# Kernel tuning notes

Measured on AMD Instinct MI355X. Metric: run time of the kernel, lower is better.

## Reference

```python
import jax, jax.numpy as jnp
import numpy as np

EPS = 1e-6
N_LEVELS = 8
BASE_RES = 16
DESIRED_RES = 128
N_POINTS = 524288


def _grid_meta():
    # replicate DAGrid.__init__ level resolutions and flat-table offsets
    b = (DESIRED_RES / BASE_RES) ** (1.0 / (N_LEVELS - 1))
    scales, offsets = [], [0]
    for i in range(N_LEVELS):
        res = int(BASE_RES * b ** i)
        scales.append(res)
        offsets.append(offsets[-1] + (res + 1) ** 3)
    return scales, offsets


def setup_inputs() -> dict:
    key = jax.random.key(0)
    scales, offsets = _grid_meta()
    lo = np.array([-1.0, -1.0, -1.0], np.float32)
    hi_eps = np.array([1.0, 1.0, 1.0], np.float32) - EPS  # bounds[1] -= eps before anchor init
    anchors = []
    for res in scales:
        axes = [np.linspace(lo[d], hi_eps[d], res + 1, dtype=np.float32) for d in range(3)]
        g = np.stack(np.meshgrid(*axes, indexing='ij'), axis=-1).reshape(-1, 3)
        anchors.append(g)
    data = jnp.asarray(np.concatenate(anchors, axis=0))  # (T, 3) learned grid param
    xyz = jax.random.normal(key, (N_POINTS, 3), dtype=jnp.float32)
    return {
        'xyz': xyz,
        'data': data,
        'scales': jnp.asarray(scales, jnp.float32),              # (L,)
        'level_offsets': jnp.asarray(offsets[:-1], jnp.int32),   # (L,)
        'bounds': jnp.asarray(np.stack([lo, np.array([1.0, 1.0, 1.0], np.float32)])),  # (2,3) raw bbox
    }


def reference(xyz, data, scales, level_offsets, bounds):
    L = scales.shape[0]
    lo = bounds[0]
    hi = bounds[1] - EPS
    size = jnp.max(bounds[1] - bounds[0])
    x = jnp.clip(xyz, lo, hi)
    xn = (x - lo) / size                                   # (N,3) in [0,1)
    fx = xn[None, :, :] * scales[:, None, None]            # (L,N,3)
    base = jnp.floor(fx).astype(jnp.int32)                 # (L,N,3) lower corner
    off = fx - base.astype(fx.dtype)                       # (L,N,3) trilinear frac
    corners = jnp.asarray([[0, 0, 0], [0, 0, 1], [0, 1, 0], [0, 1, 1],
                           [1, 0, 0], [1, 0, 1], [1, 1, 0], [1, 1, 1]], jnp.int32)  # (8,3)
    idx = base[:, :, None, :] + corners[None, None, :, :]  # (L,N,8,3)
    r1 = (scales + 1.0).astype(jnp.int32)                  # (L,) points per axis
    ind = (idx[..., 0] * (r1 * r1)[:, None, None]
           + idx[..., 1] * r1[:, None, None]
           + idx[..., 2]
           + level_offsets[:, None, None])                 # (L,N,8) flat gather index
    val = data[ind]                                        # (L,N,8,3) gathered anchors
    cf = corners.astype(fx.dtype)
    w = jnp.clip(1.0 - cf + (2.0 * cf - 1.0) * off[:, :, None, :], 0.0, 1.0)  # (L,N,8,3)
    w = w[..., 0] * w[..., 1] * w[..., 2]                  # (L,N,8) trilinear weights
    freqs = (2.0 ** jnp.arange(L, dtype=fx.dtype))[:, None, None, None]
    enc = jnp.concatenate([jnp.sin(val * freqs), jnp.cos(val * freqs)], axis=-1)  # (L,N,8,6)
    out = jnp.einsum('lnk,lnkf->nlf', w, enc)              # (N,L,6)
    out = out.reshape(xyz.shape[0], -1)                    # (N, 6*L)
    return jnp.concatenate([xyz, out], axis=-1)            # (N, 3 + 6*L)
```

## Files before the change

kernel.cpp:

```cpp
#include <hip/hip_runtime.h>

#define NLEV 8
#define PTS_PER_BLOCK 32
#define ROW_F 51

__global__ __launch_bounds__(256) void dagrid_kernel(
    const float* __restrict__ xyz,
    const float* __restrict__ data,
    const float* __restrict__ scales,
    const int*   __restrict__ level_offsets,
    const float* __restrict__ bounds,
    float* __restrict__ out,
    int npts)
{
    __shared__ float sxyz[PTS_PER_BLOCK * 3];
    __shared__ float sres[PTS_PER_BLOCK][ROW_F];

    const int tid = threadIdx.x;
    const int l   = tid & 7;
    const int p   = tid >> 3;
    const int block_base = blockIdx.x * PTS_PER_BLOCK;

    if (tid < PTS_PER_BLOCK * 3) {
        int gi = block_base * 3 + tid;
        sxyz[tid] = (gi < npts * 3) ? xyz[gi] : 0.0f;
    }
    __syncthreads();

    const int n = block_base + p;
    const bool active = (n < npts);

    const float lox = bounds[0], loy = bounds[1], loz = bounds[2];
    const float hix = bounds[3] - 1e-6f;
    const float hiy = bounds[4] - 1e-6f;
    const float hiz = bounds[5] - 1e-6f;
    const float size = fmaxf(fmaxf(bounds[3] - bounds[0], bounds[4] - bounds[1]),
                             bounds[5] - bounds[2]);
    const float inv_size = 1.0f / size;

    const float rx = sxyz[p * 3 + 0];
    const float ry = sxyz[p * 3 + 1];
    const float rz = sxyz[p * 3 + 2];

    float acc0 = 0.f, acc1 = 0.f, acc2 = 0.f, acc3 = 0.f, acc4 = 0.f, acc5 = 0.f;

    if (active) {
        const float x = fminf(fmaxf(rx, lox), hix);
        const float y = fminf(fmaxf(ry, loy), hiy);
        const float z = fminf(fmaxf(rz, loz), hiz);
        const float xn = (x - lox) * inv_size;
        const float yn = (y - loy) * inv_size;
        const float zn = (z - loz) * inv_size;

        const float scale = scales[l];
        const int off_l = level_offsets[l];
        const int r1 = (int)scale + 1;
        const int r1sq = r1 * r1;

        const float fx = xn * scale;
        const float fy = yn * scale;
        const float fz = zn * scale;
        const float bxf = floorf(fx);
        const float byf = floorf(fy);
        const float bzf = floorf(fz);
        const int bx = (int)bxf;
        const int by = (int)byf;
        const int bz = (int)bzf;
        const float ox = fx - bxf;
        const float oy = fy - byf;
        const float oz = fz - bzf;

        const int i000 = bx * r1sq + by * r1 + bz + off_l;
        const float freq = (float)(1 << l);
        const float w_z0 = 1.0f - oz;

        #pragma unroll
        for (int cx = 0; cx < 2; ++cx) {
            const float wx = cx ? ox : (1.0f - ox);
            #pragma unroll
            for (int cy = 0; cy < 2; ++cy) {
                const float wxy = wx * (cy ? oy : (1.0f - oy));
                const float w0 = wxy * w_z0;
                const float w1 = wxy * oz;
                const float* pv = data + 3 * (size_t)(i000 + cx * r1sq + cy * r1);
                const float v0x = pv[0], v0y = pv[1], v0z = pv[2];
                const float v1x = pv[3], v1y = pv[4], v1z = pv[5];

                float a;
                a = v0x * freq; acc0 += w0 * __sinf(a); acc3 += w0 * __cosf(a);
                a = v0y * freq; acc1 += w0 * __sinf(a); acc4 += w0 * __cosf(a);
                a = v0z * freq; acc2 += w0 * __sinf(a); acc5 += w0 * __cosf(a);
                a = v1x * freq; acc0 += w1 * __sinf(a); acc3 += w1 * __cosf(a);
                a = v1y * freq; acc1 += w1 * __sinf(a); acc4 += w1 * __cosf(a);
                a = v1z * freq; acc2 += w1 * __sinf(a); acc5 += w1 * __cosf(a);
            }
        }
    }

    {
        float* row = sres[p];
        const int c = 3 + l * 6;
        row[c + 0] = acc0; row[c + 1] = acc1; row[c + 2] = acc2;
        row[c + 3] = acc3; row[c + 4] = acc4; row[c + 5] = acc5;
        if (l == 0) { row[0] = rx; row[1] = ry; row[2] = rz; }
    }
    __syncthreads();

    {
        const float* flat = &sres[0][0];
        float* ob = out + (size_t)block_base * ROW_F;
        const int lim = npts * ROW_F - block_base * ROW_F;
        for (int i = tid; i < PTS_PER_BLOCK * ROW_F; i += 256) {
            if (i < lim) ob[i] = flat[i];
        }
    }
}

extern "C" void kernel_launch(void* const* d_in, const int* in_sizes, int n_in,
                              void* d_out, int out_size, void* d_ws, size_t ws_size,
                              hipStream_t stream) {
    const float* xyz           = (const float*)d_in[0];
    const float* data          = (const float*)d_in[1];
    const float* scales        = (const float*)d_in[2];
    const int*   level_offsets = (const int*)d_in[3];
    const float* bounds        = (const float*)d_in[4];
    float* out = (float*)d_out;

    const int npts = in_sizes[0] / 3;
    const int nblocks = (npts + PTS_PER_BLOCK - 1) / PTS_PER_BLOCK;
    dagrid_kernel<<<nblocks, 256, 0, stream>>>(xyz, data, scales, level_offsets,
                                               bounds, out, npts);
}
```

Baseline: 144.3 us.

## Repack grid table to float4 rows and vectorize gathers and output stores

Adds a pre-pass kernel that copies the (T,3) anchor table into a padded float4 table in workspace, so each corner pair is fetched with two 16-byte loads instead of six scalar loads. The main kernel also vectorizes the xyz load and the output store for full blocks, and uses sincos in place of separate sin and cos calls. The cost is an extra kernel launch plus a full read and write of the table (about 1.2M entries) on every call. The original scalar path is kept as a fallback for when no workspace is provided.

```diff
diff --git a/kernel.cpp b/kernel.cpp
--- a/kernel.cpp
+++ b/kernel.cpp
@@ -4,7 +4,153 @@
 #define PTS_PER_BLOCK 32
 #define ROW_F 51
 
+__global__ __launch_bounds__(256) void repack_kernel(
+    const float* __restrict__ data, float4* __restrict__ tab, int T)
+{
+    const int g = blockIdx.x * 256 + threadIdx.x;
+    const int base = g * 4;
+    if (base >= T) return;
+    if (base + 4 <= T) {
+        const float4* src = (const float4*)(data + (size_t)base * 3);
+        const float4 a = src[0], b = src[1], c = src[2];
+        tab[base + 0] = make_float4(a.x, a.y, a.z, 0.f);
+        tab[base + 1] = make_float4(a.w, b.x, b.y, 0.f);
+        tab[base + 2] = make_float4(b.z, b.w, c.x, 0.f);
+        tab[base + 3] = make_float4(c.y, c.z, c.w, 0.f);
+    } else {
+        for (int j = base; j < T; ++j)
+            tab[j] = make_float4(data[3*(size_t)j], data[3*(size_t)j+1],
+                                 data[3*(size_t)j+2], 0.f);
+    }
+}
+
 __global__ __launch_bounds__(256) void dagrid_kernel(
+    const float* __restrict__ xyz,
+    const float4* __restrict__ tab,
+    const float* __restrict__ scales,
+    const int*   __restrict__ level_offsets,
+    const float* __restrict__ bounds,
+    float* __restrict__ out,
+    int npts)
+{
+    __shared__ alignas(16) float sxyz[PTS_PER_BLOCK * 3];
+    __shared__ alignas(16) float sres[PTS_PER_BLOCK][ROW_F];
+
+    const int tid = threadIdx.x;
+    const int l   = tid & 7;
+    const int p   = tid >> 3;
+    const int block_base = blockIdx.x * PTS_PER_BLOCK;
+    const bool full_block = (block_base + PTS_PER_BLOCK <= npts);
+
+    if (full_block) {
+        if (tid < 24) {
+            ((float4*)sxyz)[tid] = ((const float4*)(xyz + (size_t)block_base * 3))[tid];
+        }
+    } else if (tid < PTS_PER_BLOCK * 3) {
+        const int gi = block_base * 3 + tid;
+        sxyz[tid] = (gi < npts * 3) ? xyz[gi] : 0.0f;
+    }
+
+    const float scale = scales[l];
+    const int   off_l = level_offsets[l];
+
+    const float lox = bounds[0], loy = bounds[1], loz = bounds[2];
+    const float hix = bounds[3] - 1e-6f;
+    const float hiy = bounds[4] - 1e-6f;
+    const float hiz = bounds[5] - 1e-6f;
+    const float size = fmaxf(fmaxf(bounds[3] - bounds[0], bounds[4] - bounds[1]),
+                             bounds[5] - bounds[2]);
+    const float inv_size = 1.0f / size;
+
+    __syncthreads();
+
+    const int n = block_base + p;
+    const bool active = (n < npts);
+
+    const float rx = sxyz[p * 3 + 0];
+    const float ry = sxyz[p * 3 + 1];
+    const float rz = sxyz[p * 3 + 2];
+
+    float acc0 = 0.f, acc1 = 0.f, acc2 = 0.f, acc3 = 0.f, acc4 = 0.f, acc5 = 0.f;
+
+    if (active) {
+        const float x = fminf(fmaxf(rx, lox), hix);
+        const float y = fminf(fmaxf(ry, loy), hiy);
+        const float z = fminf(fmaxf(rz, loz), hiz);
+        const float xn = (x - lox) * inv_size;
+        const float yn = (y - loy) * inv_size;
+        const float zn = (z - loz) * inv_size;
+
+        const int r1   = (int)scale + 1;
+        const int r1sq = r1 * r1;
+
+        const float fx = xn * scale;
+        const float fy = yn * scale;
+        const float fz = zn * scale;
+        const float bxf = floorf(fx), byf = floorf(fy), bzf = floorf(fz);
+        const float ox = fx - bxf;
+        const float oy = fy - byf;
+        const float oz = fz - bzf;
+
+        const int i000 = (int)bxf * r1sq + (int)byf * r1 + (int)bzf + off_l;
+
+        const float4* t0 = tab + i000;
+        const float4* t1 = tab + i000 + r1;
+        const float4* t2 = tab + i000 + r1sq;
+        const float4* t3 = tab + i000 + r1sq + r1;
+        const float4 A0 = t0[0], B0 = t0[1];
+        const float4 A1 = t1[0], B1 = t1[1];
+        const float4 A2 = t2[0], B2 = t2[1];
+        const float4 A3 = t3[0], B3 = t3[1];
+
+        const float freq = (float)(1 << l);
+        const float wz0  = 1.0f - oz;
+        const float wx1 = ox, wx0 = 1.0f - ox;
+        const float wy1 = oy, wy0 = 1.0f - oy;
+
+        float sn, cs;
+        #define PAIR(A, B, WXY)                                                   \
+        {                                                                         \
+            const float w0 = (WXY) * wz0;                                         \
+            const float w1 = (WXY) * oz;                                          \
+            __sincosf(A.x * freq, &sn, &cs); acc0 += w0 * sn; acc3 += w0 * cs;    \
+            __sincosf(A.y * freq, &sn, &cs); acc1 += w0 * sn; acc4 += w0 * cs;    \
+            __sincosf(A.z * freq, &sn, &cs); acc2 += w0 * sn; acc5 += w0 * cs;    \
+            __sincosf(B.x * freq, &sn, &cs); acc0 += w1 * sn; acc3 += w1 * cs;    \
+            __sincosf(B.y * freq, &sn, &cs); acc1 += w1 * sn; acc4 += w1 * cs;    \
+            __sincosf(B.z * freq, &sn, &cs); acc2 += w1 * sn; acc5 += w1 * cs;    \
+        }
+        PAIR(A0, B0, wx0 * wy0)
+        PAIR(A1, B1, wx0 * wy1)
+        PAIR(A2, B2, wx1 * wy0)
+        PAIR(A3, B3, wx1 * wy1)
+        #undef PAIR
+    }
+
+    {
+        float* row = sres[p];
+        const int c = 3 + l * 6;
+        row[c + 0] = acc0; row[c + 1] = acc1; row[c + 2] = acc2;
+        row[c + 3] = acc3; row[c + 4] = acc4; row[c + 5] = acc5;
+        if (l == 0) { row[0] = rx; row[1] = ry; row[2] = rz; }
+    }
+    __syncthreads();
+
+    if (full_block) {
+        const float4* flat4 = (const float4*)&sres[0][0];
+        float4* ob4 = (float4*)(out + (size_t)block_base * ROW_F);
+        for (int i = tid; i < (PTS_PER_BLOCK * ROW_F) / 4; i += 256)
+            ob4[i] = flat4[i];
+    } else {
+        const float* flat = &sres[0][0];
+        float* ob = out + (size_t)block_base * ROW_F;
+        const int lim = npts * ROW_F - block_base * ROW_F;
+        for (int i = tid; i < PTS_PER_BLOCK * ROW_F; i += 256)
+            if (i < lim) ob[i] = flat[i];
+    }
+}
+
+__global__ __launch_bounds__(256) void dagrid_kernel_direct(
     const float* __restrict__ xyz,
     const float* __restrict__ data,
     const float* __restrict__ scales,
@@ -25,11 +171,8 @@
         int gi = block_base * 3 + tid;
         sxyz[tid] = (gi < npts * 3) ? xyz[gi] : 0.0f;
     }
-    __syncthreads();
-
-    const int n = block_base + p;
-    const bool active = (n < npts);
-
+    const float scale = scales[l];
+    const int   off_l = level_offsets[l];
     const float lox = bounds[0], loy = bounds[1], loz = bounds[2];
     const float hix = bounds[3] - 1e-6f;
     const float hiy = bounds[4] - 1e-6f;
@@ -37,11 +180,13 @@
     const float size = fmaxf(fmaxf(bounds[3] - bounds[0], bounds[4] - bounds[1]),
                              bounds[5] - bounds[2]);
     const float inv_size = 1.0f / size;
-
+    __syncthreads();
+
+    const int n = block_base + p;
+    const bool active = (n < npts);
     const float rx = sxyz[p * 3 + 0];
     const float ry = sxyz[p * 3 + 1];
     const float rz = sxyz[p * 3 + 2];
-
     float acc0 = 0.f, acc1 = 0.f, acc2 = 0.f, acc3 = 0.f, acc4 = 0.f, acc5 = 0.f;
 
     if (active) {
@@ -51,29 +196,14 @@
         const float xn = (x - lox) * inv_size;
         const float yn = (y - loy) * inv_size;
         const float zn = (z - loz) * inv_size;
-
-        const float scale = scales[l];
-        const int off_l = level_offsets[l];
         const int r1 = (int)scale + 1;
         const int r1sq = r1 * r1;
-
-        const float fx = xn * scale;
-        const float fy = yn * scale;
-        const float fz = zn * scale;
-        const float bxf = floorf(fx);
-        const float byf = floorf(fy);
-        const float bzf = floorf(fz);
-        const int bx = (int)bxf;
-        const int by = (int)byf;
-        const int bz = (int)bzf;
-        const float ox = fx - bxf;
-        const float oy = fy - byf;
-        const float oz = fz - bzf;
-
-        const int i000 = bx * r1sq + by * r1 + bz + off_l;
+        const float fx = xn * scale, fy = yn * scale, fz = zn * scale;
+        const float bxf = floorf(fx), byf = floorf(fy), bzf = floorf(fz);
+        const float ox = fx - bxf, oy = fy - byf, oz = fz - bzf;
+        const int i000 = (int)bxf * r1sq + (int)byf * r1 + (int)bzf + off_l;
         const float freq = (float)(1 << l);
         const float w_z0 = 1.0f - oz;
-
         #pragma unroll
         for (int cx = 0; cx < 2; ++cx) {
             const float wx = cx ? ox : (1.0f - ox);
@@ -83,20 +213,16 @@
                 const float w0 = wxy * w_z0;
                 const float w1 = wxy * oz;
                 const float* pv = data + 3 * (size_t)(i000 + cx * r1sq + cy * r1);
-                const float v0x = pv[0], v0y = pv[1], v0z = pv[2];
-                const float v1x = pv[3], v1y = pv[4], v1z = pv[5];
-
-                float a;
-                a = v0x * freq; acc0 += w0 * __sinf(a); acc3 += w0 * __cosf(a);
-                a = v0y * freq; acc1 += w0 * __sinf(a); acc4 += w0 * __cosf(a);
-                a = v0z * freq; acc2 += w0 * __sinf(a); acc5 += w0 * __cosf(a);
-                a = v1x * freq; acc0 += w1 * __sinf(a); acc3 += w1 * __cosf(a);
-                a = v1y * freq; acc1 += w1 * __sinf(a); acc4 += w1 * __cosf(a);
-                a = v1z * freq; acc2 += w1 * __sinf(a); acc5 += w1 * __cosf(a);
+                float sn, cs, a;
+                a = pv[0] * freq; __sincosf(a, &sn, &cs); acc0 += w0 * sn; acc3 += w0 * cs;
+                a = pv[1] * freq; __sincosf(a, &sn, &cs); acc1 += w0 * sn; acc4 += w0 * cs;
+                a = pv[2] * freq; __sincosf(a, &sn, &cs); acc2 += w0 * sn; acc5 += w0 * cs;
+                a = pv[3] * freq; __sincosf(a, &sn, &cs); acc0 += w1 * sn; acc3 += w1 * cs;
+                a = pv[4] * freq; __sincosf(a, &sn, &cs); acc1 += w1 * sn; acc4 += w1 * cs;
+                a = pv[5] * freq; __sincosf(a, &sn, &cs); acc2 += w1 * sn; acc5 += w1 * cs;
             }
         }
     }
-
     {
         float* row = sres[p];
         const int c = 3 + l * 6;
@@ -105,14 +231,12 @@
         if (l == 0) { row[0] = rx; row[1] = ry; row[2] = rz; }
     }
     __syncthreads();
-
     {
         const float* flat = &sres[0][0];
         float* ob = out + (size_t)block_base * ROW_F;
         const int lim = npts * ROW_F - block_base * ROW_F;
-        for (int i = tid; i < PTS_PER_BLOCK * ROW_F; i += 256) {
+        for (int i = tid; i < PTS_PER_BLOCK * ROW_F; i += 256)
             if (i < lim) ob[i] = flat[i];
-        }
     }
 }
 
@@ -127,7 +251,20 @@
     float* out = (float*)d_out;
 
     const int npts = in_sizes[0] / 3;
+    const int T    = in_sizes[1] / 3;
     const int nblocks = (npts + PTS_PER_BLOCK - 1) / PTS_PER_BLOCK;
-    dagrid_kernel<<<nblocks, 256, 0, stream>>>(xyz, data, scales, level_offsets,
-                                               bounds, out, npts);
-}
+
+    const size_t ws_needed = (size_t)T * sizeof(float4);
+    if (d_ws != nullptr && ws_size >= ws_needed) {
+        float4* tab = (float4*)d_ws;
+        const int rgroups = (T + 3) / 4;
+        const int rblocks = (rgroups + 255) / 256;
+        repack_kernel<<<rblocks, 256, 0, stream>>>(data, tab, T);
+        dagrid_kernel<<<nblocks, 256, 0, stream>>>(xyz, tab, scales, level_offsets,
+                                                   bounds, out, npts);
+    } else {
+        dagrid_kernel_direct<<<nblocks, 256, 0, stream>>>(xyz, data, scales,
+                                                          level_offsets, bounds,
+                                                          out, npts);
+    }
+}
```

After: 176.9 us. 1.23x slower.
